# Kernel optimization log

Hardware: AMD Instinct MI355X
Metric: run time of the kernel (lower is better)

Reference implementation:

```python
import jax, jax.numpy as jnp
import numpy as np

B, T, M, C, H = 32, 128, 1290, 512, 8
NUM_BLOCKS = 4
MLP_LAYERS = 2
TOPK = 8


def _ln(x, g, b):
    mu = jnp.mean(x, -1, keepdims=True)
    var = jnp.mean((x - mu) ** 2, -1, keepdims=True)
    return (x - mu) / jnp.sqrt(var + 1e-5) * g + b


def setup_inputs() -> dict:
    key = jax.random.key(0)
    ks = jax.random.split(key, 12)

    def w(k, shape, s=0.02):
        return jax.random.normal(k, shape, jnp.float32) * s

    return {
        "ipts": jax.random.normal(ks[0], (B, T, C), jnp.float32),
        "memory": jax.random.normal(ks[1], (B, M, C), jnp.float32),
        "Wq": w(ks[2], (C, C)), "bq": jnp.zeros(C, jnp.float32),
        "Wk": w(ks[3], (C, C)), "bk": jnp.zeros(C, jnp.float32),
        "Wv": w(ks[4], (C, C)), "bv": jnp.zeros(C, jnp.float32),
        "Wm": w(ks[5], (C, C)), "bm": jnp.zeros(C, jnp.float32),  # shared attention_mlp layer
        "g1": jnp.ones(C, jnp.float32), "b1": jnp.zeros(C, jnp.float32),
        "g2": jnp.ones(C, jnp.float32), "b2": jnp.zeros(C, jnp.float32),
        "Wp": w(ks[6], (C, C)), "bp": jnp.zeros(C, jnp.float32),
        "rep_w": jax.random.normal(ks[7], (C,), jnp.float32),
        "Wig": w(ks[8], (C, 2 * C)), "big": jnp.zeros(2 * C, jnp.float32),
        "Wmg": w(ks[9], (C, 2 * C)), "bmg": jnp.zeros(2 * C, jnp.float32),
        "forget_bias": jnp.float32(1.0),
        "input_bias": jnp.float32(0.0),
    }


def reference(ipts, memory, Wq, bq, Wk, bk, Wv, bv, Wm, bm, g1, b1, g2, b2,
              Wp, bp, rep_w, Wig, big, Wmg, bmg, forget_bias, input_bias):
    Dh = C // H
    scale = 1.0 / np.sqrt(Dh)

    def heads(x):  # [B,L,C] -> [B,H,L,Dh]
        return x.reshape(x.shape[0], x.shape[1], H, Dh).transpose(0, 2, 1, 3)

    def mha(inp, mem, use_topk):
        # query from mem, key/value from inp (matches multi_head_attention(ipts, memory))
        q, k, v = heads(mem @ Wq + bq), heads(inp @ Wk + bk), heads(inp @ Wv + bv)
        att = jax.nn.softmax(jnp.einsum('bhqd,bhkd->bhqk', q, k) * scale, axis=-1)
        if use_topk:
            _, idx = jax.lax.top_k(att, TOPK)  # [B,H,Q,TOPK]
            mask = jnp.zeros_like(att)
            for i in range(TOPK):  # small fixed loop; avoids [.,.,.,K,L] blowup
                mask = mask + jax.nn.one_hot(idx[..., i], att.shape[-1], dtype=att.dtype)
            att = att * mask
        o = jnp.einsum('bhqk,bhkd->bhqd', att, v)
        return o.transpose(0, 2, 1, 3).reshape(o.shape[0], o.shape[2], C)

    inp = ipts @ Wp + bp  # input_projector, [B,T,C]
    mem = memory
    for _ in range(NUM_BLOCKS):
        mem = _ln(mem + mha(inp, mem, True), g1, b1)
        h = mem
        for _ in range(MLP_LAYERS):  # shared weights (ModuleList([lin]*L))
            h = jax.nn.relu(h @ Wm + bm)
        mem = _ln(mem + h, g2, b2)

    # gates (gate_style='unit')
    gi = jnp.mean(jax.nn.relu(rep_w * inp), axis=1) @ Wig + big  # [B,2C]
    gm = jnp.tanh(memory) @ Wmg + bmg                            # [B,M,2C]
    gates = gm + gi[:, None, :]
    ig = jax.nn.sigmoid(gates[..., :C] + input_bias)
    fg = jax.nn.sigmoid(gates[..., C:] + forget_bias)
    next_memory = ig * jnp.tanh(mem) + fg * memory

    # hx: query from inp, key/value from next_memory, no topk
    hx = mha(next_memory, inp, False)  # [B,T,C]
    return (next_memory, hx)
```

## Files before the change

kernel.cpp:

```cpp
#include <hip/hip_runtime.h>
#include <stdint.h>

typedef uint16_t u16;
typedef uint32_t u32;

#define DEVI __device__ __forceinline__

DEVI float b2f(u16 u) { return __uint_as_float(((u32)u) << 16); }
DEVI float blo(u32 u) { return __uint_as_float(u << 16); }
DEVI float bhi(u32 u) { return __uint_as_float(u & 0xffff0000u); }
DEVI u16 f2b(float f) {
  u32 x = __float_as_uint(f);
  return (u16)((x + 0x7fffu + ((x >> 16) & 1u)) >> 16);
}
DEVI u32 pack2(float a, float b) { return (u32)f2b(a) | ((u32)f2b(b) << 16); }
DEVI float sigm(float x) { return 1.f / (1.f + __expf(-x)); }

typedef __bf16 bf16x8 __attribute__((ext_vector_type(8)));
typedef float f32x4 __attribute__((ext_vector_type(4)));

#define MFMA16(a, b, c) __builtin_amdgcn_mfma_f32_16x16x32_bf16(a, b, c, 0, 0, 0)

DEVI void gll16(const void* g, void* l) {
  __builtin_amdgcn_global_load_lds((const __attribute__((address_space(1))) void*)g,
                                   (__attribute__((address_space(3))) void*)l, 16, 0, 0);
}

DEVI u32 fmono(float s) {
  u32 x = __float_as_uint(s);
  return x ^ (((u32)((int)x >> 31)) | 0x80000000u);
}

DEVI void ced(u32& a, u32& b) {
  u32 hi = max(a, b), lo = min(a, b);
  a = hi; b = lo;
}
DEVI void sort8_desc(u32* v) {
  ced(v[0], v[1]); ced(v[2], v[3]); ced(v[4], v[5]); ced(v[6], v[7]);
  ced(v[0], v[2]); ced(v[1], v[3]); ced(v[4], v[6]); ced(v[5], v[7]);
  ced(v[1], v[2]); ced(v[5], v[6]);
  ced(v[0], v[4]); ced(v[1], v[5]); ced(v[2], v[6]); ced(v[3], v[7]);
  ced(v[2], v[4]); ced(v[3], v[5]);
  ced(v[1], v[2]); ced(v[3], v[4]); ced(v[5], v[6]);
}
DEVI void bitonic8_desc(u32* v) {
  ced(v[0], v[4]); ced(v[1], v[5]); ced(v[2], v[6]); ced(v[3], v[7]);
  ced(v[0], v[2]); ced(v[1], v[3]); ced(v[4], v[6]); ced(v[5], v[7]);
  ced(v[0], v[1]); ced(v[2], v[3]); ced(v[4], v[5]); ced(v[6], v[7]);
}
DEVI void merge_top8(u32* a, const u32* b) {
#pragma unroll
  for (int j = 0; j < 8; ++j) a[j] = max(a[j], b[7 - j]);
  bitonic8_desc(a);
}

__global__ void detect_kernel(const u16* __restrict__ x, int* __restrict__ flag) {
  if (threadIdx.x == 0 && blockIdx.x == 0) {
    int f = 0;
    for (int i = 0; i < 64; ++i) {
      u16 u = x[2 * i];
      int e = (u >> 7) & 0xFF;
      if (e > 131) f = 1;
    }
    *flag = f;
  }
}

struct CvtArgs {
  const void* src[23];
  int aoff[23];
  int n[23];
  int total;
};

__global__ __launch_bounds__(256) void convert_fused(CvtArgs a, u16* __restrict__ arena,
                                                     const int* __restrict__ flag) {
  int e4 = (blockIdx.x * 256 + threadIdx.x) * 4;
  if (e4 >= a.total) return;
  const char* sp = (const char*)a.src[0];
  int rel = e4, cnt = a.n[0];
#pragma unroll
  for (int j = 1; j < 23; ++j)
    if (e4 >= a.aoff[j]) { sp = (const char*)a.src[j]; rel = e4 - a.aoff[j]; cnt = a.n[j]; }
  const bool f32 = (*flag != 0);
  if (rel + 3 < cnt) {
    if (f32) {
      float4 v = *(const float4*)(sp + (size_t)rel * 4);
      uint2 o;
      o.x = pack2(v.x, v.y);
      o.y = pack2(v.z, v.w);
      *(uint2*)(arena + e4) = o;
    } else {
      *(uint2*)(arena + e4) = *(const uint2*)(sp + (size_t)rel * 2);
    }
  } else {
#pragma unroll
    for (int k = 0; k < 4; ++k) {
      u16 o = 0;
      if (rel + k < cnt)
        o = f32 ? f2b(((const float*)sp)[rel + k]) : ((const u16*)sp)[rel + k];
      arena[e4 + k] = o;
    }
  }
}

__global__ void biascat_kernel(const u16* __restrict__ bq, const u16* __restrict__ bk,
                               const u16* __restrict__ bv, u16* __restrict__ bqkv,
                               u16* __restrict__ bkv) {
  int t = threadIdx.x;
  bqkv[t] = bq[t];
  bqkv[512 + t] = bk[t];
  bqkv[1024 + t] = bv[t];
  bkv[t] = bk[t];
  bkv[512 + t] = bv[t];
}

template <int ACT>
__global__ __launch_bounds__(256, 4) void gemm_bt(
    const u16* __restrict__ A, const u16* __restrict__ Bt,
    const u16* __restrict__ bias, u16* __restrict__ Co, int Mtot, int Ntot, int nby) {
  __shared__ __align__(16) u16 smem[128 * 136];
  u16* aT = smem;
  u16* bT = smem + 128 * 64;
  const int tid = threadIdx.x;
  const int lane = tid & 63;
  const int w = tid >> 6;

  const int nwg = gridDim.x;
  const int orig = blockIdx.x;
  const int xcd = orig & 7, sq = orig >> 3;
  const int qd = nwg >> 3, rm = nwg & 7;
  const int wg = (xcd < rm ? xcd * (qd + 1) : rm * (qd + 1) + (xcd - rm) * qd) + sq;
  const int m0 = (wg / nby) * 128;
  const int n0 = (wg % nby) * 128;

  const int wm = (w & 1) << 6;
  const int wn = (w >> 1) << 6;

  f32x4 acc[4][4] = {};

  const u16* ga[4];
  const u16* gb[4];
#pragma unroll
  for (int q = 0; q < 4; ++q) {
    int j = q * 256 + tid;
    int r = j >> 3, s = j & 7;
    int c = (s ^ (r & 7)) * 8;
    int ra = m0 + r;
    if (ra >= Mtot) ra = Mtot - 1;
    ga[q] = A + (size_t)ra * 512 + c;
    gb[q] = Bt + (size_t)(n0 + r) * 512 + c;
  }

  for (int ko = 0; ko < 8; ++ko) {
    const int k0 = ko * 64;
#pragma unroll
    for (int q = 0; q < 4; ++q) {
      int j = q * 256 + tid;
      gll16(ga[q] + k0, aT + j * 8);
      gll16(gb[q] + k0, bT + j * 8);
    }
    __syncthreads();
#pragma unroll
    for (int ks = 0; ks < 2; ++ks) {
      bf16x8 af[4], bfr[4];
#pragma unroll
      for (int i = 0; i < 4; ++i) {
        int cch = ks * 4 + (lane >> 4);
        int r = wm + i * 16 + (lane & 15);
        af[i] = *(const bf16x8*)(aT + (r * 8 + (cch ^ (r & 7))) * 8);
        int rn = wn + i * 16 + (lane & 15);
        bfr[i] = *(const bf16x8*)(bT + (rn * 8 + (cch ^ (rn & 7))) * 8);
      }
#pragma unroll
      for (int i = 0; i < 4; ++i)
#pragma unroll
        for (int jn = 0; jn < 4; ++jn)
          acc[i][jn] = MFMA16(af[i], bfr[jn], acc[i][jn]);
    }
    __syncthreads();
  }

  u16* st = smem;
  const int cl = lane & 15;
  const int rg = lane >> 4;
#pragma unroll
  for (int jn = 0; jn < 4; ++jn) {
    int coll = wn + jn * 16 + cl;
    float bv = b2f(bias[n0 + coll]);
#pragma unroll
    for (int i = 0; i < 4; ++i) {
      int rowb = wm + i * 16 + rg * 4;
#pragma unroll
      for (int rr = 0; rr < 4; ++rr) {
        float vv = acc[i][jn][rr] + bv;
        if (ACT) vv = fmaxf(vv, 0.f);
        st[(rowb + rr) * 136 + coll] = f2b(vv);
      }
    }
  }
  __syncthreads();
#pragma unroll
  for (int t = 0; t < 8; ++t) {
    int idx = (t * 256 + tid) * 8;
    int r = idx >> 7;
    int c = idx & 127;
    int row = m0 + r;
    if (row < Mtot) {
      uint4 v = *(const uint4*)(st + r * 136 + c);
      *(uint4*)(Co + (size_t)row * Ntot + n0 + c) = v;
    }
  }
}

__global__ __launch_bounds__(256) void transpose_kernel(const u16* __restrict__ in,
                                                        u16* __restrict__ outb, int K, int N) {
  __shared__ u16 tile[32][33];
  const int tx = threadIdx.x & 31, ty = threadIdx.x >> 5;
  const int bx = blockIdx.x * 32;
  const int by = blockIdx.y * 32;
#pragma unroll
  for (int i = 0; i < 32; i += 8) tile[ty + i][tx] = in[(size_t)(by + ty + i) * N + bx + tx];
  __syncthreads();
#pragma unroll
  for (int i = 0; i < 32; i += 8) outb[(size_t)(bx + ty + i) * K + by + tx] = tile[tx][ty + i];
}

__global__ void tanhmem_kernel(const u16* __restrict__ mi, u16* __restrict__ th, int n8) {
  int i = blockIdx.x * 256 + threadIdx.x;
  if (i >= n8) return;
  uint4 u = ((const uint4*)mi)[i];
  uint4 t;
  t.x = pack2(tanhf(blo(u.x)), tanhf(bhi(u.x)));
  t.y = pack2(tanhf(blo(u.y)), tanhf(bhi(u.y)));
  t.z = pack2(tanhf(blo(u.z)), tanhf(bhi(u.z)));
  t.w = pack2(tanhf(blo(u.w)), tanhf(bhi(u.w)));
  ((uint4*)th)[i] = t;
}

__global__ void redmean_kernel(const u16* __restrict__ inp, const u16* __restrict__ repw,
                               u16* __restrict__ outb) {
  const int b = blockIdx.x;
  const int c = blockIdx.y * 256 + threadIdx.x;
  const float rw = b2f(repw[c]);
  float s = 0.f;
  for (int t = 0; t < 128; ++t)
    s += fmaxf(rw * b2f(inp[(size_t)(b * 128 + t) * 512 + c]), 0.f);
  outb[b * 512 + c] = f2b(s * (1.f / 128.f));
}

__global__ __launch_bounds__(64) void ln_kernel(const u16* __restrict__ src,
                                                const u16* __restrict__ addb,
                                                u16* __restrict__ dst,
                                                const u16* __restrict__ g,
                                                const u16* __restrict__ bb) {
  const int row = blockIdx.x;
  const int lane = threadIdx.x;
  const u16* srow = src + (size_t)row * 512;
  const u16* arow = addb + (size_t)row * 512;
  float x[8];
  float s = 0.f;
#pragma unroll
  for (int i = 0; i < 8; ++i) {
    int c = lane + i * 64;
    x[i] = b2f(srow[c]) + b2f(arow[c]);
    s += x[i];
  }
#pragma unroll
  for (int off = 32; off > 0; off >>= 1) s += __shfl_xor(s, off, 64);
  const float mu = s * (1.f / 512.f);
  float v = 0.f;
#pragma unroll
  for (int i = 0; i < 8; ++i) {
    float d = x[i] - mu;
    v = fmaf(d, d, v);
  }
#pragma unroll
  for (int off = 32; off > 0; off >>= 1) v += __shfl_xor(v, off, 64);
  const float rstd = rsqrtf(v * (1.f / 512.f) + 1e-5f);
  u16* orow = dst + (size_t)row * 512;
#pragma unroll
  for (int i = 0; i < 8; ++i) {
    int c = lane + i * 64;
    orow[c] = f2b(fmaf((x[i] - mu) * rstd, b2f(g[c]), b2f(bb[c])));
  }
}

__global__ __launch_bounds__(256, 3) void attn1_mfma(const u16* __restrict__ q,
                                                     const u16* __restrict__ kb,
                                                     const u16* __restrict__ vb,
                                                     u16* __restrict__ o, int ldkv) {
  __shared__ __align__(16) u16 Pl[128 * 136];
  __shared__ __align__(16) u16 VT[64 * 136];
  __shared__ float lbuf[128];
  u16* Kl = Pl;

  const int tid = threadIdx.x;
  const int lane = tid & 63;
  const int w = tid >> 6;
  const int quad = lane >> 4;
  const int l15 = lane & 15;
  const int qb = blockIdx.x;
  const int bh = blockIdx.y;
  const int b = bh >> 3, h = bh & 7;

#pragma unroll
  for (int qq = 0; qq < 4; ++qq) {
    int j = qq * 256 + tid;
    int r = j >> 3, s = j & 7;
    gll16(kb + (size_t)(b * 128 + r) * ldkv + h * 64 + (s ^ (r & 7)) * 8, Kl + j * 8);
  }
#pragma unroll
  for (int p = 0; p < 4; ++p) {
    int key = (tid & 63) + 64 * (p & 1);
    int dc = w + 4 * (p >> 1);
    uint4 u = *(const uint4*)(vb + (size_t)(b * 128 + key) * ldkv + h * 64 + dc * 8);
    u16 tmp[8];
    *(uint4*)tmp = u;
#pragma unroll
    for (int jj = 0; jj < 8; ++jj) VT[(dc * 8 + jj) * 136 + key] = tmp[jj];
  }

  bf16x8 bq[2][2];
  {
    int ra = min(qb * 128 + w * 32 + l15, 1289);
    int rb_ = min(qb * 128 + w * 32 + 16 + l15, 1289);
    const u16* qa = q + (size_t)(b * 1290 + ra) * 512 + h * 64 + quad * 8;
    const u16* qc = q + (size_t)(b * 1290 + rb_) * 512 + h * 64 + quad * 8;
    bq[0][0] = *(const bf16x8*)(qa);
    bq[0][1] = *(const bf16x8*)(qa + 32);
    bq[1][0] = *(const bf16x8*)(qc);
    bq[1][1] = *(const bf16x8*)(qc + 32);
  }
  __syncthreads();

  f32x4 sa[2][8] = {};
#pragma unroll
  for (int ks = 0; ks < 2; ++ks) {
#pragma unroll
    for (int jn = 0; jn < 8; ++jn) {
      int n = jn * 16 + l15;
      int cch = ks * 4 + quad;
      bf16x8 ak = *(const bf16x8*)(Kl + (n * 8 + (cch ^ (n & 7))) * 8);
      sa[0][jn] = MFMA16(ak, bq[0][ks], sa[0][jn]);
      sa[1][jn] = MFMA16(ak, bq[1][ks], sa[1][jn]);
    }
  }
  __syncthreads();

  const u32 ibase = 127u - (u32)(quad * 4);
#pragma unroll
  for (int i = 0; i < 2; ++i) {
    const int qi = w * 32 + i * 16 + l15;
    u32 g[4][8];
#pragma unroll
    for (int jn = 0; jn < 8; ++jn)
#pragma unroll
      for (int rr = 0; rr < 4; ++rr) {
        float s = sa[i][jn][rr] * 0.125f;
        sa[i][jn][rr] = s;
        g[jn >> 1][(jn & 1) * 4 + rr] =
            (fmono(s) & 0xFFFFFF80u) | (ibase - (u32)(jn * 16 + rr));
      }
    sort8_desc(g[0]); sort8_desc(g[1]); sort8_desc(g[2]); sort8_desc(g[3]);
    merge_top8(g[0], g[1]);
    merge_top8(g[2], g[3]);
    merge_top8(g[0], g[2]);
    u32* tv = g[0];
#pragma unroll
    for (int off = 16; off < 64; off <<= 1) {
      u32 pv[8];
#pragma unroll
      for (int j = 0; j < 8; ++j) pv[j] = (u32)__shfl_xor((int)tv[7 - j], off, 64);
#pragma unroll
      for (int j = 0; j < 8; ++j) tv[j] = max(tv[j], pv[j]);
      bitonic8_desc(tv);
    }
    const u32 t8 = tv[7];
    u32 mb = tv[0] & 0xFFFFFF80u;
    u32 xm = (mb & 0x80000000u) ? (mb ^ 0x80000000u) : ~mb;
    const float mx = __uint_as_float(xm);
    float lsum = 0.f;
#pragma unroll
    for (int jn = 0; jn < 8; ++jn) {
      u16 pr[4];
#pragma unroll
      for (int rr = 0; rr < 4; ++rr) {
        float s = sa[i][jn][rr];
        float e = __expf(s - mx);
        lsum += e;
        u32 kk = (fmono(s) & 0xFFFFFF80u) | (ibase - (u32)(jn * 16 + rr));
        pr[rr] = (kk >= t8) ? f2b(e) : (u16)0;
      }
      uint2 st;
      st.x = (u32)pr[0] | ((u32)pr[1] << 16);
      st.y = (u32)pr[2] | ((u32)pr[3] << 16);
      *(uint2*)(Pl + qi * 136 + jn * 16 + quad * 4) = st;
    }
    lsum += __shfl_xor(lsum, 16, 64);
    lsum += __shfl_xor(lsum, 32, 64);
    if (quad == 0) lbuf[qi] = 1.f / lsum;
  }
  __syncthreads();

  f32x4 oa[2][4] = {};
#pragma unroll
  for (int kc = 0; kc < 4; ++kc) {
    bf16x8 ap[2];
#pragma unroll
    for (int i = 0; i < 2; ++i)
      ap[i] = *(const bf16x8*)(Pl + (w * 32 + i * 16 + l15) * 136 + kc * 32 + quad * 8);
#pragma unroll
    for (int jd = 0; jd < 4; ++jd) {
      bf16x8 bv_ = *(const bf16x8*)(VT + (jd * 16 + l15) * 136 + kc * 32 + quad * 8);
      oa[0][jd] = MFMA16(ap[0], bv_, oa[0][jd]);
      oa[1][jd] = MFMA16(ap[1], bv_, oa[1][jd]);
    }
  }

#pragma unroll
  for (int i = 0; i < 2; ++i) {
    int rowl = w * 32 + i * 16 + quad * 4;
#pragma unroll
    for (int rr = 0; rr < 4; ++rr) {
      int qg = qb * 128 + rowl + rr;
      if (qg < 1290) {
        float il = lbuf[rowl + rr];
        u16* orow = o + (size_t)(b * 1290 + qg) * 512 + h * 64;
#pragma unroll
        for (int jd = 0; jd < 4; ++jd) orow[jd * 16 + l15] = f2b(oa[i][jd][rr] * il);
      }
    }
  }
}

__global__ __launch_bounds__(256, 2) void attn2_mfma(const u16* __restrict__ q2,
                                                     const u16* __restrict__ k2,
                                                     const u16* __restrict__ v2,
                                                     float* __restrict__ pacc,
                                                     float* __restrict__ pml,
                                                     int ldq, int ldkv) {
  __shared__ __align__(16) u16 Kl[64 * 64];
  __shared__ __align__(16) u16 VT[64 * 72];
  __shared__ __align__(16) u16 Pl[4 * 32 * 72];
  const int tid = threadIdx.x;
  const int lane = tid & 63;
  const int w = tid >> 6;
  const int quad = lane >> 4;
  const int l15 = lane & 15;
  const int bh = blockIdx.x;
  const int b = bh >> 3, h = bh & 7;
  const int part = blockIdx.y;
  const int kstart = (part * 1290) >> 2;
  const int kend = ((part + 1) * 1290) >> 2;

  bf16x8 aq[2][2];
  {
    int r0 = b * 128 + w * 32 + l15;
    const u16* qa = q2 + (size_t)r0 * ldq + h * 64 + quad * 8;
    aq[0][0] = *(const bf16x8*)(qa);
    aq[0][1] = *(const bf16x8*)(qa + 32);
    aq[1][0] = *(const bf16x8*)(qa + (size_t)16 * ldq);
    aq[1][1] = *(const bf16x8*)(qa + (size_t)16 * ldq + 32);
  }

  f32x4 oa[2][4] = {};
  float m_[2][4], l_[2][4];
#pragma unroll
  for (int i = 0; i < 2; ++i)
#pragma unroll
    for (int r = 0; r < 4; ++r) { m_[i][r] = -1e30f; l_[i][r] = 0.f; }

  const int nk = kend - kstart;
  for (int kt = 0; kt < nk; kt += 64) {
    __syncthreads();
#pragma unroll
    for (int qq = 0; qq < 2; ++qq) {
      int j = qq * 256 + tid;
      int r = j >> 3, s = j & 7;
      int kg = kstart + kt + r;
      if (kg >= kend) kg = kend - 1;
      gll16(k2 + (size_t)(b * 1290 + kg) * ldkv + h * 64 + (s ^ (r & 7)) * 8, Kl + j * 8);
    }
    {
      int r = tid & 63;
      int kg = kstart + kt + r;
      if (kg >= kend) kg = kend - 1;
      const u16* vrow = v2 + (size_t)(b * 1290 + kg) * ldkv + h * 64;
#pragma unroll
      for (int p = 0; p < 2; ++p) {
        int dc = (tid >> 6) + p * 4;
        uint4 u = *(const uint4*)(vrow + dc * 8);
        u16 tmp[8];
        *(uint4*)tmp = u;
#pragma unroll
        for (int jj = 0; jj < 8; ++jj) VT[(dc * 8 + jj) * 72 + r] = tmp[jj];
      }
    }
    __syncthreads();

    f32x4 sa[2][4] = {};
#pragma unroll
    for (int ks = 0; ks < 2; ++ks) {
#pragma unroll
      for (int jn = 0; jn < 4; ++jn) {
        int n = jn * 16 + l15;
        int cch = ks * 4 + quad;
        bf16x8 bk = *(const bf16x8*)(Kl + (n * 8 + (cch ^ (n & 7))) * 8);
        sa[0][jn] = MFMA16(aq[0][ks], bk, sa[0][jn]);
        sa[1][jn] = MFMA16(aq[1][ks], bk, sa[1][jn]);
      }
    }

    u16* pw = Pl + w * (32 * 72);
#pragma unroll
    for (int i = 0; i < 2; ++i) {
      float rmax[4] = {-1e30f, -1e30f, -1e30f, -1e30f};
#pragma unroll
      for (int jn = 0; jn < 4; ++jn) {
        int kg = kstart + kt + jn * 16 + l15;
        bool val = kg < kend;
#pragma unroll
        for (int r = 0; r < 4; ++r) {
          float s = sa[i][jn][r] * 0.125f;
          s = val ? s : -1e30f;
          sa[i][jn][r] = s;
          rmax[r] = fmaxf(rmax[r], s);
        }
      }
#pragma unroll
      for (int off = 1; off < 16; off <<= 1)
#pragma unroll
        for (int r = 0; r < 4; ++r) rmax[r] = fmaxf(rmax[r], __shfl_xor(rmax[r], off, 64));
      float alpha[4];
#pragma unroll
      for (int r = 0; r < 4; ++r) {
        float mn = fmaxf(m_[i][r], rmax[r]);
        alpha[r] = __expf(m_[i][r] - mn);
        m_[i][r] = mn;
      }
      float lsum[4] = {0.f, 0.f, 0.f, 0.f};
#pragma unroll
      for (int jn = 0; jn < 4; ++jn)
#pragma unroll
        for (int r = 0; r < 4; ++r) {
          float p = __expf(sa[i][jn][r] - m_[i][r]);
          sa[i][jn][r] = p;
          lsum[r] += p;
        }
#pragma unroll
      for (int off = 1; off < 16; off <<= 1)
#pragma unroll
        for (int r = 0; r < 4; ++r) lsum[r] += __shfl_xor(lsum[r], off, 64);
#pragma unroll
      for (int r = 0; r < 4; ++r) l_[i][r] = l_[i][r] * alpha[r] + lsum[r];
#pragma unroll
      for (int jd = 0; jd < 4; ++jd)
#pragma unroll
        for (int r = 0; r < 4; ++r) oa[i][jd][r] *= alpha[r];
#pragma unroll
      for (int jn = 0; jn < 4; ++jn) {
        int col = jn * 16 + l15;
#pragma unroll
        for (int r = 0; r < 4; ++r)
          pw[(i * 16 + quad * 4 + r) * 72 + col] = f2b(sa[i][jn][r]);
      }
    }

#pragma unroll
    for (int ks = 0; ks < 2; ++ks) {
      bf16x8 ap[2];
#pragma unroll
      for (int i = 0; i < 2; ++i)
        ap[i] = *(const bf16x8*)(pw + (i * 16 + l15) * 72 + ks * 32 + quad * 8);
#pragma unroll
      for (int jd = 0; jd < 4; ++jd) {
        bf16x8 bv_ = *(const bf16x8*)(VT + (jd * 16 + l15) * 72 + ks * 32 + quad * 8);
        oa[0][jd] = MFMA16(ap[0], bv_, oa[0][jd]);
        oa[1][jd] = MFMA16(ap[1], bv_, oa[1][jd]);
      }
    }
  }

  float* pa = pacc + (size_t)(part * 256 + bh) * 128 * 64;
#pragma unroll
  for (int i = 0; i < 2; ++i) {
    int row = w * 32 + i * 16 + quad * 4;
#pragma unroll
    for (int r = 0; r < 4; ++r)
#pragma unroll
      for (int jd = 0; jd < 4; ++jd)
        pa[(size_t)(row + r) * 64 + jd * 16 + l15] = oa[i][jd][r];
    if (l15 == 0) {
#pragma unroll
      for (int r = 0; r < 4; ++r) {
        size_t pi = (size_t)(part * 256 + bh) * 128 + row + r;
        pml[pi * 2 + 0] = m_[i][r];
        pml[pi * 2 + 1] = l_[i][r];
      }
    }
  }
}

__global__ __launch_bounds__(64) void attn2_merge(const float* __restrict__ pacc,
                                                  const float* __restrict__ pml,
                                                  void* __restrict__ outp,
                                                  const int* __restrict__ flag) {
  const int qi = blockIdx.x;
  const int bh = qi >> 7, t = qi & 127;
  const int b = bh >> 3, h = bh & 7;
  const int lane = threadIdx.x;
  float mv[4], lv[4];
  float m0 = -1e30f;
#pragma unroll
  for (int i = 0; i < 4; ++i) {
    size_t pi = (size_t)(i * 256 + bh) * 128 + t;
    mv[i] = pml[pi * 2];
    lv[i] = pml[pi * 2 + 1];
    m0 = fmaxf(m0, mv[i]);
  }
  float L = 0.f, accd = 0.f;
#pragma unroll
  for (int i = 0; i < 4; ++i) {
    size_t pi = (size_t)(i * 256 + bh) * 128 + t;
    float e = __expf(mv[i] - m0);
    L += lv[i] * e;
    accd += pacc[pi * 64 + lane] * e;
  }
  float v = accd / L;
  size_t off = (size_t)41280 * 512 + ((size_t)(b * 128 + t) * 512 + h * 64 + lane);
  if (*flag) ((float*)outp)[off] = v; else ((u16*)outp)[off] = f2b(v);
}

__global__ __launch_bounds__(512) void gates_fused(const u16* __restrict__ gm,
                                                   const u16* __restrict__ gi,
                                                   const u16* __restrict__ memfin,
                                                   const u16* __restrict__ mem_in,
                                                   const u16* __restrict__ ibp,
                                                   const u16* __restrict__ fbp,
                                                   u16* __restrict__ nmbf,
                                                   void* __restrict__ outp,
                                                   const int* __restrict__ flag) {
  const int r = blockIdx.x;
  const int b = r / 1290;
  const int c = threadIdx.x;
  size_t i1024 = (size_t)r * 1024;
  size_t idx = (size_t)r * 512 + c;
  float ig = sigm(b2f(gm[i1024 + c]) + b2f(gi[b * 1024 + c]) + b2f(ibp[0]));
  float fg = sigm(b2f(gm[i1024 + 512 + c]) + b2f(gi[b * 1024 + 512 + c]) + b2f(fbp[0]));
  float v = ig * tanhf(b2f(memfin[idx])) + fg * b2f(mem_in[idx]);
  nmbf[idx] = f2b(v);
  if (*flag) ((float*)outp)[idx] = v; else ((u16*)outp)[idx] = f2b(v);
}

extern "C" void kernel_launch(void* const* d_in, const int* in_sizes, int n_in,
                              void* d_out, int out_size, void* d_ws, size_t ws_size,
                              hipStream_t stream) {
  (void)out_size; (void)ws_size;
  char* ws = (char*)d_ws;
  size_t off = 0;
  auto alloc = [&](size_t bytes) {
    char* p = ws + off;
    off += (bytes + 255) & ~(size_t)255;
    return (void*)p;
  };

  int* flag = (int*)alloc(256);

  size_t aoffs[32];
  size_t total = 0;
  for (int i = 0; i < n_in; ++i) {
    aoffs[i] = total;
    total += ((size_t)in_sizes[i] + 127) & ~(size_t)127;
  }
  u16* arena = (u16*)alloc(total * 2);

  const u16* c_ipts = arena + aoffs[0];
  const u16* c_mem  = arena + aoffs[1];
  const u16* c_Wq = arena + aoffs[2];  const u16* c_bq = arena + aoffs[3];
  const u16* c_Wk = arena + aoffs[4];  const u16* c_bk = arena + aoffs[5];
  const u16* c_Wv = arena + aoffs[6];  const u16* c_bv = arena + aoffs[7];
  const u16* c_Wm = arena + aoffs[8];  const u16* c_bm = arena + aoffs[9];
  const u16* c_g1 = arena + aoffs[10]; const u16* c_b1 = arena + aoffs[11];
  const u16* c_g2 = arena + aoffs[12]; const u16* c_b2 = arena + aoffs[13];
  const u16* c_Wp = arena + aoffs[14]; const u16* c_bp = arena + aoffs[15];
  const u16* c_repw = arena + aoffs[16];
  const u16* c_Wig = arena + aoffs[17]; const u16* c_big = arena + aoffs[18];
  const u16* c_Wmg = arena + aoffs[19]; const u16* c_bmg = arena + aoffs[20];
  const u16* c_fb = arena + aoffs[21];
  const u16* c_ib = arena + aoffs[22];

  u16* WqkvT = (u16*)alloc((size_t)1536 * 512 * 2);
  u16* WmT = (u16*)alloc(512 * 512 * 2);
  u16* WpT = (u16*)alloc(512 * 512 * 2);
  u16* WigT = (u16*)alloc(512 * 1024 * 2);
  u16* WmgT = (u16*)alloc(512 * 1024 * 2);
  u16* bqkv = (u16*)alloc(1536 * 2);
  u16* bkv = (u16*)alloc(1024 * 2);
  u16* inp = (u16*)alloc((size_t)4096 * 512 * 2);
  u16* qkvbuf = (u16*)alloc((size_t)4096 * 1536 * 2);
  u16* rmean = (u16*)alloc(32 * 512 * 2);
  u16* gi = (u16*)alloc(32 * 1024 * 2);
  u16* membf = (u16*)alloc((size_t)41280 * 512 * 2);
  u16* qbuf = (u16*)alloc((size_t)41280 * 512 * 2);
  u16* obuf = (u16*)alloc((size_t)41280 * 512 * 2);
  u16* gmbuf = (u16*)alloc((size_t)41280 * 512 * 2);
  u16* nmbf = (u16*)alloc((size_t)41280 * 512 * 2);
  (void)gmbuf;
  u16* gm1024 = obuf;
  u16* kvbuf = obuf;
  float* pacc = (float*)(void*)qbuf;
  float* pml = (float*)((char*)(void*)qbuf + (size_t)4 * 32768 * 64 * 4);

  detect_kernel<<<1, 64, 0, stream>>>((const u16*)d_in[0], flag);
  {
    CvtArgs ca;
    for (int i = 0; i < 23; ++i) {
      int ii = (i < n_in) ? i : (n_in - 1);
      ca.src[i] = d_in[ii];
      ca.aoff[i] = (int)aoffs[ii];
      ca.n[i] = in_sizes[ii];
    }
    ca.total = (int)total;
    convert_fused<<<(unsigned)((total / 4 + 255) / 256), 256, 0, stream>>>(ca, arena, flag);
  }
  biascat_kernel<<<1, 512, 0, stream>>>(c_bq, c_bk, c_bv, bqkv, bkv);

  transpose_kernel<<<dim3(16, 16), 256, 0, stream>>>(c_Wq, WqkvT, 512, 512);
  transpose_kernel<<<dim3(16, 16), 256, 0, stream>>>(c_Wk, WqkvT + (size_t)512 * 512, 512, 512);
  transpose_kernel<<<dim3(16, 16), 256, 0, stream>>>(c_Wv, WqkvT + (size_t)1024 * 512, 512, 512);
  transpose_kernel<<<dim3(16, 16), 256, 0, stream>>>(c_Wm, WmT, 512, 512);
  transpose_kernel<<<dim3(16, 16), 256, 0, stream>>>(c_Wp, WpT, 512, 512);
  transpose_kernel<<<dim3(32, 16), 256, 0, stream>>>(c_Wig, WigT, 512, 1024);
  transpose_kernel<<<dim3(32, 16), 256, 0, stream>>>(c_Wmg, WmgT, 512, 1024);

  gemm_bt<0><<<dim3(32 * 4), 256, 0, stream>>>(c_ipts, WpT, c_bp, inp, 4096, 512, 4);
  gemm_bt<0><<<dim3(32 * 12), 256, 0, stream>>>(inp, WqkvT, bqkv, qkvbuf, 4096, 1536, 12);

  redmean_kernel<<<dim3(32, 2), 256, 0, stream>>>(inp, c_repw, rmean);
  gemm_bt<0><<<dim3(1 * 8), 256, 0, stream>>>(rmean, WigT, c_big, gi, 32, 1024, 8);

  const u16* memsrc = c_mem;
  for (int it = 0; it < 4; ++it) {
    gemm_bt<0><<<dim3(323 * 4), 256, 0, stream>>>(memsrc, WqkvT, c_bq, qbuf, 41280, 512, 4);
    attn1_mfma<<<dim3(11, 256), 256, 0, stream>>>(qbuf, qkvbuf + 512, qkvbuf + 1024, obuf, 1536);
    ln_kernel<<<dim3(41280), 64, 0, stream>>>(memsrc, obuf, membf, c_g1, c_b1);
    gemm_bt<1><<<dim3(323 * 4), 256, 0, stream>>>(membf, WmT, c_bm, qbuf, 41280, 512, 4);
    gemm_bt<1><<<dim3(323 * 4), 256, 0, stream>>>(qbuf, WmT, c_bm, obuf, 41280, 512, 4);
    ln_kernel<<<dim3(41280), 64, 0, stream>>>(membf, obuf, membf, c_g2, c_b2);
    memsrc = membf;
  }

  tanhmem_kernel<<<dim3(2641920 / 256), 256, 0, stream>>>(c_mem, qbuf, 2641920);
  gemm_bt<0><<<dim3(323 * 8), 256, 0, stream>>>(qbuf, WmgT, c_bmg, gm1024, 41280, 1024, 8);
  gates_fused<<<dim3(41280), 512, 0, stream>>>(gm1024, gi, membf, c_mem, c_ib, c_fb,
                                               nmbf, d_out, flag);

  gemm_bt<0><<<dim3(323 * 8), 256, 0, stream>>>(nmbf, WqkvT + (size_t)512 * 512, bkv,
                                                kvbuf, 41280, 1024, 8);
  attn2_mfma<<<dim3(256, 4), 256, 0, stream>>>(qkvbuf, kvbuf, kvbuf + 512, pacc, pml,
                                               1536, 1024);
  attn2_merge<<<dim3(32768), 64, 0, stream>>>(pacc, pml, d_out, flag);
}
```

Baseline: 1.215 ms.

## Fuse gate GEMM with gating epilogue and use fast exp-based tanh

Replaces the separate gate GEMM and elementwise gates kernel with a single GEMM whose tiles pair the matching input-gate and forget-gate column blocks, so the sigmoid/tanh combine runs in the epilogue straight from shared memory. This removes the round trip of the [41280,1024] gate activations through global memory and one kernel launch. tanhf is also replaced by an exp-based approximation in both the tanh kernel and the new epilogue. The exp-based form trades a little accuracy for cheaper math.

```diff
diff --git a/kernel.cpp b/kernel.cpp
--- a/kernel.cpp
+++ b/kernel.cpp
@@ -15,6 +15,7 @@
 }
 DEVI u32 pack2(float a, float b) { return (u32)f2b(a) | ((u32)f2b(b) << 16); }
 DEVI float sigm(float x) { return 1.f / (1.f + __expf(-x)); }
+DEVI float ftanh(float x) { return 1.f - 2.f / (1.f + __expf(2.f * x)); }
 
 typedef __bf16 bf16x8 __attribute__((ext_vector_type(8)));
 typedef float f32x4 __attribute__((ext_vector_type(4)));
@@ -213,6 +214,145 @@
   }
 }
 
+__global__ __launch_bounds__(256, 4) void gemm_gates(
+    const u16* __restrict__ A, const u16* __restrict__ WmgTp,
+    const u16* __restrict__ bmg, const u16* __restrict__ gi,
+    const u16* __restrict__ memfin, const u16* __restrict__ mem_in,
+    const u16* __restrict__ ibp, const u16* __restrict__ fbp,
+    u16* __restrict__ nmbf, void* __restrict__ outp, const int* __restrict__ flag,
+    int Mtot) {
+  __shared__ __align__(16) u16 smem[128 * 136];
+  u16* aT = smem;
+  u16* bT = smem + 128 * 64;
+  const int tid = threadIdx.x;
+  const int lane = tid & 63;
+  const int w = tid >> 6;
+
+  const int nwg = gridDim.x;
+  const int orig = blockIdx.x;
+  const int xcd = orig & 7, sq = orig >> 3;
+  const int qd = nwg >> 3, rm = nwg & 7;
+  const int wg = (xcd < rm ? xcd * (qd + 1) : rm * (qd + 1) + (xcd - rm) * qd) + sq;
+  const int m0 = (wg >> 3) * 128;
+  const int n0h = (wg & 7) * 64;
+
+  const int wm = (w & 1) << 6;
+  const int wn = (w >> 1) << 6;
+
+  f32x4 acc[4][4] = {};
+
+  const u16* ga[4];
+  const u16* gb[4];
+#pragma unroll
+  for (int q = 0; q < 4; ++q) {
+    int j = q * 256 + tid;
+    int r = j >> 3, s = j & 7;
+    int c = (s ^ (r & 7)) * 8;
+    int ra = m0 + r;
+    if (ra >= Mtot) ra = Mtot - 1;
+    ga[q] = A + (size_t)ra * 512 + c;
+    int br = (r < 64) ? (n0h + r) : (512 + n0h + r - 64);
+    gb[q] = WmgTp + (size_t)br * 512 + c;
+  }
+
+  for (int ko = 0; ko < 8; ++ko) {
+    const int k0 = ko * 64;
+#pragma unroll
+    for (int q = 0; q < 4; ++q) {
+      int j = q * 256 + tid;
+      gll16(ga[q] + k0, aT + j * 8);
+      gll16(gb[q] + k0, bT + j * 8);
+    }
+    __syncthreads();
+#pragma unroll
+    for (int ks = 0; ks < 2; ++ks) {
+      bf16x8 af[4], bfr[4];
+#pragma unroll
+      for (int i = 0; i < 4; ++i) {
+        int cch = ks * 4 + (lane >> 4);
+        int r = wm + i * 16 + (lane & 15);
+        af[i] = *(const bf16x8*)(aT + (r * 8 + (cch ^ (r & 7))) * 8);
+        int rn = wn + i * 16 + (lane & 15);
+        bfr[i] = *(const bf16x8*)(bT + (rn * 8 + (cch ^ (rn & 7))) * 8);
+      }
+#pragma unroll
+      for (int i = 0; i < 4; ++i)
+#pragma unroll
+        for (int jn = 0; jn < 4; ++jn)
+          acc[i][jn] = MFMA16(af[i], bfr[jn], acc[i][jn]);
+    }
+    __syncthreads();
+  }
+
+  u16* st = smem;
+  const int cl = lane & 15;
+  const int rg = lane >> 4;
+#pragma unroll
+  for (int jn = 0; jn < 4; ++jn) {
+    int coll = wn + jn * 16 + cl;
+    int bcol = (coll < 64) ? (n0h + coll) : (512 + n0h + coll - 64);
+    float bv = b2f(bmg[bcol]);
+#pragma unroll
+    for (int i = 0; i < 4; ++i) {
+      int rowb = wm + i * 16 + rg * 4;
+#pragma unroll
+      for (int rr = 0; rr < 4; ++rr)
+        st[(rowb + rr) * 136 + coll] = f2b(acc[i][jn][rr] + bv);
+    }
+  }
+  __syncthreads();
+
+  const float ib = b2f(ibp[0]);
+  const float fb = b2f(fbp[0]);
+  const bool of32 = (*flag != 0);
+#pragma unroll
+  for (int t = 0; t < 4; ++t) {
+    int chunk = t * 256 + tid;
+    int rl = chunk >> 3;
+    int c8 = (chunk & 7) * 8;
+    int row = m0 + rl;
+    if (row >= Mtot) continue;
+    int b = row / 1290;
+    size_t gidx = (size_t)row * 512 + n0h + c8;
+    uint4 uig = *(const uint4*)(st + rl * 136 + c8);
+    uint4 ufg = *(const uint4*)(st + rl * 136 + 64 + c8);
+    uint4 ugi = *(const uint4*)(gi + b * 1024 + n0h + c8);
+    uint4 ugf = *(const uint4*)(gi + b * 1024 + 512 + n0h + c8);
+    uint4 umf = *(const uint4*)(memfin + gidx);
+    uint4 umi = *(const uint4*)(mem_in + gidx);
+    const u32* pig = (const u32*)&uig;
+    const u32* pfg = (const u32*)&ufg;
+    const u32* pgi = (const u32*)&ugi;
+    const u32* pgf = (const u32*)&ugf;
+    const u32* pmf = (const u32*)&umf;
+    const u32* pmi = (const u32*)&umi;
+    float v[8];
+#pragma unroll
+    for (int k = 0; k < 4; ++k) {
+      float ig0 = sigm(blo(pig[k]) + blo(pgi[k]) + ib);
+      float ig1 = sigm(bhi(pig[k]) + bhi(pgi[k]) + ib);
+      float fg0 = sigm(blo(pfg[k]) + blo(pgf[k]) + fb);
+      float fg1 = sigm(bhi(pfg[k]) + bhi(pgf[k]) + fb);
+      v[2 * k] = ig0 * ftanh(blo(pmf[k])) + fg0 * blo(pmi[k]);
+      v[2 * k + 1] = ig1 * ftanh(bhi(pmf[k])) + fg1 * bhi(pmi[k]);
+    }
+    uint4 o;
+    u32* po = (u32*)&o;
+#pragma unroll
+    for (int k = 0; k < 4; ++k) po[k] = pack2(v[2 * k], v[2 * k + 1]);
+    *(uint4*)(nmbf + gidx) = o;
+    if (of32) {
+      float4 f0, f1;
+      f0.x = v[0]; f0.y = v[1]; f0.z = v[2]; f0.w = v[3];
+      f1.x = v[4]; f1.y = v[5]; f1.z = v[6]; f1.w = v[7];
+      *(float4*)((float*)outp + gidx) = f0;
+      *(float4*)((float*)outp + gidx + 4) = f1;
+    } else {
+      *(uint4*)((u16*)outp + gidx) = o;
+    }
+  }
+}
+
 __global__ __launch_bounds__(256) void transpose_kernel(const u16* __restrict__ in,
                                                         u16* __restrict__ outb, int K, int N) {
   __shared__ u16 tile[32][33];
@@ -231,10 +371,10 @@
   if (i >= n8) return;
   uint4 u = ((const uint4*)mi)[i];
   uint4 t;
-  t.x = pack2(tanhf(blo(u.x)), tanhf(bhi(u.x)));
-  t.y = pack2(tanhf(blo(u.y)), tanhf(bhi(u.y)));
-  t.z = pack2(tanhf(blo(u.z)), tanhf(bhi(u.z)));
-  t.w = pack2(tanhf(blo(u.w)), tanhf(bhi(u.w)));
+  t.x = pack2(ftanh(blo(u.x)), ftanh(bhi(u.x)));
+  t.y = pack2(ftanh(blo(u.y)), ftanh(bhi(u.y)));
+  t.z = pack2(ftanh(blo(u.z)), ftanh(bhi(u.z)));
+  t.w = pack2(ftanh(blo(u.w)), ftanh(bhi(u.w)));
   ((uint4*)th)[i] = t;
 }
 
@@ -632,27 +772,6 @@
   if (*flag) ((float*)outp)[off] = v; else ((u16*)outp)[off] = f2b(v);
 }
 
-__global__ __launch_bounds__(512) void gates_fused(const u16* __restrict__ gm,
-                                                   const u16* __restrict__ gi,
-                                                   const u16* __restrict__ memfin,
-                                                   const u16* __restrict__ mem_in,
-                                                   const u16* __restrict__ ibp,
-                                                   const u16* __restrict__ fbp,
-                                                   u16* __restrict__ nmbf,
-                                                   void* __restrict__ outp,
-                                                   const int* __restrict__ flag) {
-  const int r = blockIdx.x;
-  const int b = r / 1290;
-  const int c = threadIdx.x;
-  size_t i1024 = (size_t)r * 1024;
-  size_t idx = (size_t)r * 512 + c;
-  float ig = sigm(b2f(gm[i1024 + c]) + b2f(gi[b * 1024 + c]) + b2f(ibp[0]));
-  float fg = sigm(b2f(gm[i1024 + 512 + c]) + b2f(gi[b * 1024 + 512 + c]) + b2f(fbp[0]));
-  float v = ig * tanhf(b2f(memfin[idx])) + fg * b2f(mem_in[idx]);
-  nmbf[idx] = f2b(v);
-  if (*flag) ((float*)outp)[idx] = v; else ((u16*)outp)[idx] = f2b(v);
-}
-
 extern "C" void kernel_launch(void* const* d_in, const int* in_sizes, int n_in,
                               void* d_out, int out_size, void* d_ws, size_t ws_size,
                               hipStream_t stream) {
@@ -707,7 +826,6 @@
   u16* gmbuf = (u16*)alloc((size_t)41280 * 512 * 2);
   u16* nmbf = (u16*)alloc((size_t)41280 * 512 * 2);
   (void)gmbuf;
-  u16* gm1024 = obuf;
   u16* kvbuf = obuf;
   float* pacc = (float*)(void*)qbuf;
   float* pml = (float*)((char*)(void*)qbuf + (size_t)4 * 32768 * 64 * 4);
@@ -752,9 +870,8 @@
   }
 
   tanhmem_kernel<<<dim3(2641920 / 256), 256, 0, stream>>>(c_mem, qbuf, 2641920);
-  gemm_bt<0><<<dim3(323 * 8), 256, 0, stream>>>(qbuf, WmgT, c_bmg, gm1024, 41280, 1024, 8);
-  gates_fused<<<dim3(41280), 512, 0, stream>>>(gm1024, gi, membf, c_mem, c_ib, c_fb,
-                                               nmbf, d_out, flag);
+  gemm_gates<<<dim3(323 * 8), 256, 0, stream>>>(qbuf, WmgT, c_bmg, gi, membf, c_mem,
+                                                c_ib, c_fb, nmbf, d_out, flag, 41280);
 
   gemm_bt<0><<<dim3(323 * 8), 256, 0, stream>>>(nmbf, WqkvT + (size_t)512 * 512, bkv,
                                                 kvbuf, 41280, 1024, 8);
```

Result: slower. 1.246 ms (+2.6%).
